# Optimization experiments

Hardware: AMD Instinct MI355X
Metric: run time of the kernel (lower is better)

## Reference

```python
import jax, jax.numpy as jnp
import numpy as np

POOL = 2  # pooling_size == pooling_stride == 2, SAME padding, H even -> no actual pad


def setup_inputs() -> dict:
    key = jax.random.key(0)
    k1, k2 = jax.random.split(key)
    B, H, C = 8, 28, 32
    mu_in = jax.random.normal(k1, (B, H, H, C), dtype=jnp.float32)
    # per-channel spatial covariance: [B, H*H, H*H, C]
    Sigma_in = jax.random.uniform(k2, (B, H * H, H * H, C), dtype=jnp.float32)
    return {"mu_in": mu_in, "Sigma_in": Sigma_in}


def reference(mu_in, Sigma_in):
    B, H, W, C = mu_in.shape
    ho, wo = H // POOL, W // POOL
    # non-overlapping 2x2 windows, row-major within window (matches TF argmax order)
    patches = mu_in.reshape(B, ho, POOL, wo, POOL, C).transpose(0, 1, 3, 2, 4, 5)
    patches = patches.reshape(B, ho, wo, POOL * POOL, C)
    mu_out = jnp.max(patches, axis=3)                     # [B, ho, wo, C]
    k = jnp.argmax(patches, axis=3)                       # [B, ho, wo, C], first-match ties like TF
    dy, dx = k // POOL, k % POOL
    iy = POOL * jnp.arange(ho)[None, :, None, None] + dy  # input row of the max
    ix = POOL * jnp.arange(wo)[None, None, :, None] + dx  # input col of the max
    # TF decode: index = y*hw_in + x  (flat spatial index in the input image)
    index = (iy * W + ix).astype(jnp.int32)               # [B, ho, wo, C]
    index = index.transpose(0, 3, 1, 2).reshape(B, C, ho * wo)  # [B, C, N_out]
    # Sigma: [B, N_in, N_in, C] -> [B, C, N_in, N_in], then double gather
    S1 = Sigma_in.transpose(0, 3, 1, 2)
    g1 = jnp.take_along_axis(S1, index[:, :, :, None], axis=2)       # [B, C, N_out, N_in]
    Sigma_out = jnp.take_along_axis(g1, index[:, :, None, :], axis=3)  # [B, C, N_out, N_out]
    Sigma_out = Sigma_out.transpose(0, 2, 3, 1)           # [B, N_out, N_out, C]
    return mu_out, Sigma_out
```

## Files before the change

### kernel.cpp

```cpp
#include <hip/hip_runtime.h>
#include <stdint.h>

#define BATCH 8
#define HIN   28
#define CH    32
#define HO    14
#define NIN   784
#define NOUT  196
#define JHALF 392
#define HTILE (98 * CH)
#define NITEM (4 * JHALF * 8)
#define UNROLL 7
#define OUTER  (NITEM / 256 / UNROLL)

typedef float f32x4 __attribute__((ext_vector_type(4)));

__global__ __launch_bounds__(256, 6) void vdp_pool_half_kernel(
        const float* __restrict__ mu_in,
        const float* __restrict__ sigma_in,
        float* __restrict__ mu_out,
        float* __restrict__ sigma_out)
{
    __shared__ __align__(16) float out_tile[HTILE + 64];
    __shared__ uint32_t cmq[JHALF * 2];
    __shared__ uint32_t pmask[2];

    const int bid = blockIdx.x;
    const int qh  = bid & 1;
    const int bp  = bid >> 1;
    const int b   = bp / NOUT;
    const int p   = bp - b * NOUT;
    const int tid = threadIdx.x;
    const int py  = p / HO, px = p - py * HO;

    if (tid < 198) {
        const int isP = (tid >= 196);
        int qy, qx, hf, ql;
        if (isP) { hf = tid - 196; qy = py; qx = px; ql = 0; }
        else     { ql = tid >> 1; hf = tid & 1;
                   const int qyl = ql / HO; qx = ql - qyl * HO; qy = qh * 7 + qyl; }

        const float* base =
            mu_in + (((size_t)b * HIN + 2 * qy) * HIN + 2 * qx) * CH + hf * 16;

        uint32_t kqh = 0;
        float mu4[4][4];
        #pragma unroll
        for (int g = 0; g < 4; ++g) {
            const float4 v0 = *(const float4*)(base + g * 4);
            const float4 v1 = *(const float4*)(base + CH + g * 4);
            const float4 v2 = *(const float4*)(base + HIN * CH + g * 4);
            const float4 v3 = *(const float4*)(base + HIN * CH + CH + g * 4);
            #pragma unroll
            for (int m = 0; m < 4; ++m) {
                const float e0 = (&v0.x)[m], e1 = (&v1.x)[m],
                            e2 = (&v2.x)[m], e3 = (&v3.x)[m];
                float best = e0; uint32_t k = 0;
                if (e1 > best) { best = e1; k = 1; }
                if (e2 > best) { best = e2; k = 2; }
                if (e3 > best) { best = e3; k = 3; }
                mu4[g][m] = best;
                kqh |= k << (2 * (g * 4 + m));
            }
        }
        if (isP) {
            pmask[hf] = kqh;
            if (((py < 7) ? 0 : 1) == qh) {
                #pragma unroll
                for (int g = 0; g < 4; ++g)
                    *(float4*)(mu_out + (size_t)bp * CH + hf * 16 + g * 4) =
                        make_float4(mu4[g][0], mu4[g][1], mu4[g][2], mu4[g][3]);
            }
        } else {
            const int jbl = (2 * qy) * HIN + 2 * qx - qh * JHALF;
            const uint32_t qb = (uint32_t)(ql * CH) << 16;
            #pragma unroll
            for (int dj = 0; dj < 4; ++dj) {
                uint32_t mm = 0;
                #pragma unroll
                for (int cl = 0; cl < 16; ++cl)
                    mm |= (((kqh >> (2 * cl)) & 3u) == (uint32_t)dj)
                          ? (1u << cl) : 0u;
                const int jl = jbl + (dj >> 1) * HIN + (dj & 1);
                cmq[jl * 2 + hf] = qb | mm;
            }
        }
    }
    __syncthreads();

    const uint32_t e      = (uint32_t)tid & 7u;
    const uint32_t half16 = e >> 2;
    const uint32_t shs    = (e & 3u) * 4u;
    const uint32_t hw     = e * 4u;
    const uint32_t posb   = (uint32_t)tid >> 3;
    const uint32_t ibase  = (uint32_t)(2 * py) * HIN + 2u * px;
    const uint32_t trash  = HTILE + ((uint32_t)tid & 63u);

    const uint32_t pm = pmask[half16];
    unsigned long long rmpack = 0ull;
    #pragma unroll
    for (int r = 0; r < 4; ++r) {
        uint32_t mm = 0;
        #pragma unroll
        for (int cl = 0; cl < 16; ++cl)
            mm |= (((pm >> (2 * cl)) & 3u) == (uint32_t)r) ? (1u << cl) : 0u;
        rmpack |= (unsigned long long)mm << (16 * r);
    }

    const float* sb = sigma_in + (size_t)b * NIN * NIN * CH
                    + (size_t)qh * JHALF * CH;
    for (int o = 0; o < OUTER; ++o) {
        f32x4    val[UNROLL];
        uint32_t tab[UNROLL];
        uint32_t rmv[UNROLL];
        #pragma unroll
        for (int u = 0; u < UNROLL; ++u) {
            const uint32_t pos = (uint32_t)(o * UNROLL + u) * 32u + posb;
            const uint32_t r   = pos / JHALF;
            const uint32_t jl  = pos - r * JHALF;
            const uint32_t i   = ibase + (r >> 1) * HIN + (r & 1u);
            val[u] = __builtin_nontemporal_load(
                (const f32x4*)(sb + ((size_t)i * NIN + jl) * CH + hw));
            tab[u] = cmq[jl * 2 + half16];
            rmv[u] = (uint32_t)(rmpack >> (r * 16u)) & 0xFFFFu;
        }
        #pragma unroll
        for (int u = 0; u < UNROLL; ++u) {
            const uint32_t sel16 = rmv[u] & (tab[u] & 0xFFFFu);
            const uint32_t s4    = (sel16 >> shs) & 0xFu;
            const uint32_t bs    = (tab[u] >> 16) + hw;
            out_tile[(s4 & 1u) ? bs + 0u : trash] = val[u][0];
            out_tile[(s4 & 2u) ? bs + 1u : trash] = val[u][1];
            out_tile[(s4 & 4u) ? bs + 2u : trash] = val[u][2];
            out_tile[(s4 & 8u) ? bs + 3u : trash] = val[u][3];
        }
    }
    __syncthreads();

    {
        const f32x4* srcT = (const f32x4*)out_tile;
        f32x4* dstT = (f32x4*)(sigma_out + (size_t)bp * (NOUT * CH)
                               + (size_t)qh * HTILE);
        for (int w = tid; w < HTILE / 4; w += 256)
            __builtin_nontemporal_store(srcT[w], &dstT[w]);
    }
}

extern "C" void kernel_launch(void* const* d_in, const int* in_sizes, int n_in,
                              void* d_out, int out_size, void* d_ws, size_t ws_size,
                              hipStream_t stream) {
    const float* mu_in    = (const float*)d_in[0];
    const float* sigma_in = (const float*)d_in[1];

    float* mu_out    = (float*)d_out;
    float* sigma_out = (float*)d_out + BATCH * NOUT * CH;

    vdp_pool_half_kernel<<<BATCH * NOUT * 2, 256, 0, stream>>>(
        mu_in, sigma_in, mu_out, sigma_out);
}
```

Measured before the change: 124.5 us.

## Precompute pooling masks in a separate kernel instead of per block

Moves the max-pool argmax and mask construction out of the main gather kernel into a small prepass kernel that writes the column-mask table and row masks to workspace. Each gather block now just copies the precomputed table into shared memory rather than redoing 198 threads of mu_in loads and compares. This removes a lot of duplicated computation across the 3136 blocks, but adds a second kernel launch and a global-memory round trip for the tables.

```diff
diff --git a/kernel.cpp b/kernel.cpp
--- a/kernel.cpp
+++ b/kernel.cpp
@@ -9,21 +9,82 @@
 #define NOUT  196
 #define JHALF 392
 #define HTILE (98 * CH)
-#define NITEM (4 * JHALF * 8)
 #define UNROLL 7
-#define OUTER  (NITEM / 256 / UNROLL)
+#define OUTER  7
 
 typedef float f32x4 __attribute__((ext_vector_type(4)));
 
+__global__ void vdp_mask_kernel(const float* __restrict__ mu_in,
+                                float* __restrict__ mu_out,
+                                uint32_t* __restrict__ cmq_g,
+                                unsigned long long* __restrict__ rm_g) {
+    const int t = blockIdx.x * 256 + threadIdx.x;
+    if (t >= BATCH * NOUT * 2) return;
+    const int hf = t & 1;
+    const int bq = t >> 1;
+    const int q  = bq % NOUT;
+    const int b  = bq / NOUT;
+    const int qy = q / HO, qx = q - qy * HO;
+
+    const float* base =
+        mu_in + (((size_t)b * HIN + 2 * qy) * HIN + 2 * qx) * CH + hf * 16;
+
+    uint32_t kqh = 0;
+    #pragma unroll
+    for (int g = 0; g < 4; ++g) {
+        const float4 v0 = *(const float4*)(base + g * 4);
+        const float4 v1 = *(const float4*)(base + CH + g * 4);
+        const float4 v2 = *(const float4*)(base + HIN * CH + g * 4);
+        const float4 v3 = *(const float4*)(base + HIN * CH + CH + g * 4);
+        float mu4[4];
+        #pragma unroll
+        for (int m = 0; m < 4; ++m) {
+            const float e0 = (&v0.x)[m], e1 = (&v1.x)[m],
+                        e2 = (&v2.x)[m], e3 = (&v3.x)[m];
+            float best = e0; uint32_t k = 0;
+            if (e1 > best) { best = e1; k = 1; }
+            if (e2 > best) { best = e2; k = 2; }
+            if (e3 > best) { best = e3; k = 3; }
+            mu4[m] = best;
+            kqh |= k << (2 * (g * 4 + m));
+        }
+        *(float4*)(mu_out + (size_t)bq * CH + hf * 16 + g * 4) =
+            make_float4(mu4[0], mu4[1], mu4[2], mu4[3]);
+    }
+
+    const int ql = q - ((qy >= 7) ? 98 : 0);
+    const uint32_t qb = (uint32_t)(ql * CH) << 16;
+    const int jb = (2 * qy) * HIN + 2 * qx;
+    #pragma unroll
+    for (int dj = 0; dj < 4; ++dj) {
+        uint32_t mm = 0;
+        #pragma unroll
+        for (int cl = 0; cl < 16; ++cl)
+            mm |= (((kqh >> (2 * cl)) & 3u) == (uint32_t)dj) ? (1u << cl) : 0u;
+        const int j = jb + (dj >> 1) * HIN + (dj & 1);
+        cmq_g[((size_t)b * NIN + j) * 2 + hf] = qb | mm;
+    }
+
+    unsigned long long rmpack = 0ull;
+    #pragma unroll
+    for (int r = 0; r < 4; ++r) {
+        uint32_t mm = 0;
+        #pragma unroll
+        for (int cl = 0; cl < 16; ++cl)
+            mm |= (((kqh >> (2 * cl)) & 3u) == (uint32_t)r) ? (1u << cl) : 0u;
+        rmpack |= (unsigned long long)mm << (16 * r);
+    }
+    rm_g[(size_t)bq * 2 + hf] = rmpack;
+}
+
 __global__ __launch_bounds__(256, 6) void vdp_pool_half_kernel(
-        const float* __restrict__ mu_in,
         const float* __restrict__ sigma_in,
-        float* __restrict__ mu_out,
+        const uint32_t* __restrict__ cmq_g,
+        const unsigned long long* __restrict__ rm_g,
         float* __restrict__ sigma_out)
 {
     __shared__ __align__(16) float out_tile[HTILE + 64];
     __shared__ uint32_t cmq[JHALF * 2];
-    __shared__ uint32_t pmask[2];
 
     const int bid = blockIdx.x;
     const int qh  = bid & 1;
@@ -33,79 +94,24 @@
     const int tid = threadIdx.x;
     const int py  = p / HO, px = p - py * HO;
 
-    if (tid < 198) {
-        const int isP = (tid >= 196);
-        int qy, qx, hf, ql;
-        if (isP) { hf = tid - 196; qy = py; qx = px; ql = 0; }
-        else     { ql = tid >> 1; hf = tid & 1;
-                   const int qyl = ql / HO; qx = ql - qyl * HO; qy = qh * 7 + qyl; }
-
-        const float* base =
-            mu_in + (((size_t)b * HIN + 2 * qy) * HIN + 2 * qx) * CH + hf * 16;
-
-        uint32_t kqh = 0;
-        float mu4[4][4];
+    {
+        const uint32_t* src = cmq_g + ((size_t)b * NIN + qh * JHALF) * 2;
         #pragma unroll
-        for (int g = 0; g < 4; ++g) {
-            const float4 v0 = *(const float4*)(base + g * 4);
-            const float4 v1 = *(const float4*)(base + CH + g * 4);
-            const float4 v2 = *(const float4*)(base + HIN * CH + g * 4);
-            const float4 v3 = *(const float4*)(base + HIN * CH + CH + g * 4);
-            #pragma unroll
-            for (int m = 0; m < 4; ++m) {
-                const float e0 = (&v0.x)[m], e1 = (&v1.x)[m],
-                            e2 = (&v2.x)[m], e3 = (&v3.x)[m];
-                float best = e0; uint32_t k = 0;
-                if (e1 > best) { best = e1; k = 1; }
-                if (e2 > best) { best = e2; k = 2; }
-                if (e3 > best) { best = e3; k = 3; }
-                mu4[g][m] = best;
-                kqh |= k << (2 * (g * 4 + m));
-            }
-        }
-        if (isP) {
-            pmask[hf] = kqh;
-            if (((py < 7) ? 0 : 1) == qh) {
-                #pragma unroll
-                for (int g = 0; g < 4; ++g)
-                    *(float4*)(mu_out + (size_t)bp * CH + hf * 16 + g * 4) =
-                        make_float4(mu4[g][0], mu4[g][1], mu4[g][2], mu4[g][3]);
-            }
-        } else {
-            const int jbl = (2 * qy) * HIN + 2 * qx - qh * JHALF;
-            const uint32_t qb = (uint32_t)(ql * CH) << 16;
-            #pragma unroll
-            for (int dj = 0; dj < 4; ++dj) {
-                uint32_t mm = 0;
-                #pragma unroll
-                for (int cl = 0; cl < 16; ++cl)
-                    mm |= (((kqh >> (2 * cl)) & 3u) == (uint32_t)dj)
-                          ? (1u << cl) : 0u;
-                const int jl = jbl + (dj >> 1) * HIN + (dj & 1);
-                cmq[jl * 2 + hf] = qb | mm;
-            }
+        for (int k = 0; k < 4; ++k) {
+            const int w = tid + k * 256;
+            if (w < JHALF * 2) cmq[w] = src[w];
         }
     }
+    const uint32_t half16 = ((uint32_t)tid >> 2) & 1u;
+    const unsigned long long rmpack = rm_g[(size_t)bp * 2 + half16];
     __syncthreads();
 
-    const uint32_t e      = (uint32_t)tid & 7u;
-    const uint32_t half16 = e >> 2;
-    const uint32_t shs    = (e & 3u) * 4u;
-    const uint32_t hw     = e * 4u;
-    const uint32_t posb   = (uint32_t)tid >> 3;
-    const uint32_t ibase  = (uint32_t)(2 * py) * HIN + 2u * px;
-    const uint32_t trash  = HTILE + ((uint32_t)tid & 63u);
-
-    const uint32_t pm = pmask[half16];
-    unsigned long long rmpack = 0ull;
-    #pragma unroll
-    for (int r = 0; r < 4; ++r) {
-        uint32_t mm = 0;
-        #pragma unroll
-        for (int cl = 0; cl < 16; ++cl)
-            mm |= (((pm >> (2 * cl)) & 3u) == (uint32_t)r) ? (1u << cl) : 0u;
-        rmpack |= (unsigned long long)mm << (16 * r);
-    }
+    const uint32_t e     = (uint32_t)tid & 7u;
+    const uint32_t shs   = (e & 3u) * 4u;
+    const uint32_t hw    = e * 4u;
+    const uint32_t posb  = (uint32_t)tid >> 3;
+    const uint32_t ibase = (uint32_t)(2 * py) * HIN + 2u * px;
+    const uint32_t trash = HTILE + ((uint32_t)tid & 63u);
 
     const float* sb = sigma_in + (size_t)b * NIN * NIN * CH
                     + (size_t)qh * JHALF * CH;
@@ -155,6 +161,15 @@
     float* mu_out    = (float*)d_out;
     float* sigma_out = (float*)d_out + BATCH * NOUT * CH;
 
+    uint32_t* cmq_g = (uint32_t*)d_ws;
+    unsigned long long* rm_g =
+        (unsigned long long*)((char*)d_ws + BATCH * NIN * 2 * sizeof(uint32_t));
+
+    {
+        const int total = BATCH * NOUT * 2;
+        vdp_mask_kernel<<<(total + 255) / 256, 256, 0, stream>>>(
+            mu_in, mu_out, cmq_g, rm_g);
+    }
     vdp_pool_half_kernel<<<BATCH * NOUT * 2, 256, 0, stream>>>(
-        mu_in, sigma_in, mu_out, sigma_out);
+        sigma_in, cmq_g, rm_g, sigma_out);
 }
```

Result: faster. 117.4 us (-5.7%).
